# Performance work log

Hardware: AMD Instinct MI355X
Metric: run time of the kernel (lower is better)

Reference implementation:

```python
import jax, jax.numpy as jnp
import numpy as np

B, TE, TD, HE, HD = 4, 512, 256, 128, 256

def setup_inputs() -> dict:
    key = jax.random.key(0)
    k1, k2, k3, k4, k5 = jax.random.split(key, 5)
    return {
        "encoder_out_seq": jax.random.normal(k1, (B, TE, HE), dtype=jnp.float32),
        "decoder_out_seq": jax.random.normal(k2, (B, TD, HD), dtype=jnp.float32),
        "W_a": jax.random.normal(k3, (HE, HE), dtype=jnp.float32) * 0.05,
        "U_a": jax.random.normal(k4, (HD, HE), dtype=jnp.float32) * 0.05,
        "V_a": jax.random.normal(k5, (HE, 1), dtype=jnp.float32) * 0.05,
    }

def reference(encoder_out_seq, decoder_out_seq, W_a, U_a, V_a):
    # Bahdanau additive attention, fully parallel over decoder steps
    # (the original K.rnn scan has no true recurrence: each step is independent).
    Ws = jnp.einsum('bse,ef->bsf', encoder_out_seq, W_a)   # [B,Te,He]
    Uh = jnp.einsum('btd,df->btf', decoder_out_seq, U_a)   # [B,Td,He]
    # [B,Td,Te,He] additive score features
    feat = jnp.tanh(Ws[:, None, :, :] + Uh[:, :, None, :])
    e = jnp.einsum('btsf,f->bts', feat, V_a[:, 0])         # [B,Td,Te]
    e = jax.nn.softmax(e, axis=-1)                         # attention weights
    c = jnp.einsum('bts,bse->bte', e, encoder_out_seq)     # [B,Td,He] contexts
    return (c, e)
```

## Files before the change

kernel.cpp:

```cpp
#include <hip/hip_runtime.h>

#define Bn  4
#define TEn 512
#define TDn 256
#define HEn 128
#define HDn 256

__device__ __forceinline__ float tanh_fast(float x) {
    float e = __expf(2.0f * x);
    return 1.0f - 2.0f * __builtin_amdgcn_rcpf(e + 1.0f);
}

__global__ __launch_bounds__(512) void ws_gemm_kernel(
    const float* __restrict__ enc, const float* __restrict__ W,
    float* __restrict__ Ws)
{
    __shared__ __align__(16) float enc_lds[4 * HEn];
    const int tid = threadIdx.x;
    const int c   = tid & (HEn - 1);
    const int rl  = tid >> 7;
    const int r0  = blockIdx.x * 4;
    enc_lds[tid] = enc[r0 * HEn + tid];
    __syncthreads();
    const float* wc = W + c;
    const float* er = enc_lds + rl * HEn;
    float acc = 0.f;
    #pragma unroll 4
    for (int k = 0; k < HEn; k += 8) {
        float4 e0 = *(const float4*)(er + k);
        float4 e1 = *(const float4*)(er + k + 4);
        acc = fmaf(e0.x, wc[(k + 0) * HEn], acc);
        acc = fmaf(e0.y, wc[(k + 1) * HEn], acc);
        acc = fmaf(e0.z, wc[(k + 2) * HEn], acc);
        acc = fmaf(e0.w, wc[(k + 3) * HEn], acc);
        acc = fmaf(e1.x, wc[(k + 4) * HEn], acc);
        acc = fmaf(e1.y, wc[(k + 5) * HEn], acc);
        acc = fmaf(e1.z, wc[(k + 6) * HEn], acc);
        acc = fmaf(e1.w, wc[(k + 7) * HEn], acc);
    }
    Ws[(r0 + rl) * HEn + c] = acc;
}

__global__ __launch_bounds__(512, 4) void attn_kernel(
    const float* __restrict__ enc, const float* __restrict__ dec,
    const float* __restrict__ U, const float* __restrict__ V,
    const float* __restrict__ Ws, float* __restrict__ c_out,
    float* __restrict__ e_out)
{
    const int bp   = blockIdx.x;
    const int b    = bp >> 7;
    const int t0   = (bp & 127) * 2;
    const int bt0  = b * TDn + t0;
    const int tid  = threadIdx.x;
    const int lane = tid & 63;
    const int wave = tid >> 6;

    __shared__ __align__(16) float dec_lds[2 * HDn];
    __shared__ __align__(16) float uh0[HEn];
    __shared__ __align__(16) float uh1[HEn];
    __shared__ __align__(16) float part[32][HEn];
    __shared__ __align__(16) float sc0[TEn];
    __shared__ __align__(16) float sc1[TEn];
    __shared__ float redm[2][8];
    __shared__ float reds[2][8];

    dec_lds[tid] = dec[bt0 * HDn + tid];
    __syncthreads();

    {
        const int f = tid & 127;
        const int p = tid >> 7;
        const float* d0 = dec_lds + p * 64;
        const float* d1 = dec_lds + HDn + p * 64;
        const float* u  = U + (p * 64) * HEn + f;
        float a0 = 0.f, a1 = 0.f;
        #pragma unroll 8
        for (int k = 0; k < 64; ++k) {
            const float uk = u[k * HEn];
            a0 = fmaf(d0[k], uk, a0);
            a1 = fmaf(d1[k], uk, a1);
        }
        part[p][f]     = a0;
        part[4 + p][f] = a1;
    }
    __syncthreads();
    if (tid < HEn)
        uh0[tid] = part[0][tid] + part[1][tid] + part[2][tid] + part[3][tid];
    else if (tid < 2 * HEn) {
        const int f = tid - HEn;
        uh1[f] = part[4][f] + part[5][f] + part[6][f] + part[7][f];
    }
    __syncthreads();

    {
        const int s_sub = lane & 7;
        const int f0    = (lane >> 3) * 16;
        float4 vv[4], u0[4], u1[4];
        #pragma unroll
        for (int j = 0; j < 4; ++j) {
            vv[j] = *(const float4*)(V   + f0 + 4 * j);
            u0[j] = *(const float4*)(uh0 + f0 + 4 * j);
            u1[j] = *(const float4*)(uh1 + f0 + 4 * j);
        }
        const float* wsb = Ws + (b * TEn + wave * 64) * HEn;
        #pragma unroll 2
        for (int ci = 0; ci < 8; ++ci) {
            const float* wp = wsb + (ci * 8 + s_sub) * HEn + f0;
            float x0 = 0.f, x1 = 0.f;
            #pragma unroll
            for (int j = 0; j < 4; ++j) {
                float4 w = ((const float4*)wp)[j];
                x0 = fmaf(vv[j].x, tanh_fast(w.x + u0[j].x), x0);
                x1 = fmaf(vv[j].x, tanh_fast(w.x + u1[j].x), x1);
                x0 = fmaf(vv[j].y, tanh_fast(w.y + u0[j].y), x0);
                x1 = fmaf(vv[j].y, tanh_fast(w.y + u1[j].y), x1);
                x0 = fmaf(vv[j].z, tanh_fast(w.z + u0[j].z), x0);
                x1 = fmaf(vv[j].z, tanh_fast(w.z + u1[j].z), x1);
                x0 = fmaf(vv[j].w, tanh_fast(w.w + u0[j].w), x0);
                x1 = fmaf(vv[j].w, tanh_fast(w.w + u1[j].w), x1);
            }
            x0 += __shfl_xor(x0, 8, 64);
            x1 += __shfl_xor(x1, 8, 64);
            x0 += __shfl_xor(x0, 16, 64);
            x1 += __shfl_xor(x1, 16, 64);
            x0 += __shfl_xor(x0, 32, 64);
            x1 += __shfl_xor(x1, 32, 64);
            if (lane < 8) {
                sc0[wave * 64 + ci * 8 + lane] = x0;
                sc1[wave * 64 + ci * 8 + lane] = x1;
            }
        }
    }
    __syncthreads();

    const float v0 = sc0[tid];
    const float v1 = sc1[tid];
    float m0 = v0, m1 = v1;
    #pragma unroll
    for (int off = 32; off; off >>= 1) {
        m0 = fmaxf(m0, __shfl_xor(m0, off, 64));
        m1 = fmaxf(m1, __shfl_xor(m1, off, 64));
    }
    if (lane == 0) { redm[0][wave] = m0; redm[1][wave] = m1; }
    __syncthreads();
    float bm0 = redm[0][0], bm1 = redm[1][0];
    #pragma unroll
    for (int w = 1; w < 8; ++w) {
        bm0 = fmaxf(bm0, redm[0][w]);
        bm1 = fmaxf(bm1, redm[1][w]);
    }
    const float ex0 = __expf(v0 - bm0);
    const float ex1 = __expf(v1 - bm1);
    float s0 = ex0, s1 = ex1;
    #pragma unroll
    for (int off = 32; off; off >>= 1) {
        s0 += __shfl_xor(s0, off, 64);
        s1 += __shfl_xor(s1, off, 64);
    }
    if (lane == 0) { reds[0][wave] = s0; reds[1][wave] = s1; }
    __syncthreads();
    float bs0 = reds[0][0], bs1 = reds[1][0];
    #pragma unroll
    for (int w = 1; w < 8; ++w) { bs0 += reds[0][w]; bs1 += reds[1][w]; }
    const float e0 = ex0 * __builtin_amdgcn_rcpf(bs0);
    const float e1 = ex1 * __builtin_amdgcn_rcpf(bs1);
    e_out[bt0 * TEn + tid]       = e0;
    e_out[(bt0 + 1) * TEn + tid] = e1;
    sc0[tid] = e0;
    sc1[tid] = e1;
    __syncthreads();

    {
        const int hl = tid & 31;
        const int sp = tid >> 5;
        const float* eb = enc + (b * TEn + sp * 32) * HEn + hl * 4;
        const float* p0 = sc0 + sp * 32;
        const float* p1 = sc1 + sp * 32;
        float4 a0 = {0.f, 0.f, 0.f, 0.f};
        float4 a1 = {0.f, 0.f, 0.f, 0.f};
        #pragma unroll 4
        for (int i = 0; i < 32; ++i) {
            const float w0 = p0[i];
            const float w1 = p1[i];
            const float4 ev = *(const float4*)(eb + i * HEn);
            a0.x = fmaf(w0, ev.x, a0.x);  a1.x = fmaf(w1, ev.x, a1.x);
            a0.y = fmaf(w0, ev.y, a0.y);  a1.y = fmaf(w1, ev.y, a1.y);
            a0.z = fmaf(w0, ev.z, a0.z);  a1.z = fmaf(w1, ev.z, a1.z);
            a0.w = fmaf(w0, ev.w, a0.w);  a1.w = fmaf(w1, ev.w, a1.w);
        }
        *(float4*)&part[sp][hl * 4]      = a0;
        *(float4*)&part[16 + sp][hl * 4] = a1;
    }
    __syncthreads();
    if (tid < 2 * HEn) {
        const int tsel = tid >> 7;
        const int h    = tid & 127;
        float s = 0.f;
        #pragma unroll
        for (int p = 0; p < 16; ++p) s += part[tsel * 16 + p][h];
        c_out[(bt0 + tsel) * HEn + h] = s;
    }
}

extern "C" void kernel_launch(void* const* d_in, const int* in_sizes, int n_in,
                              void* d_out, int out_size, void* d_ws, size_t ws_size,
                              hipStream_t stream) {
    const float* enc = (const float*)d_in[0];
    const float* dec = (const float*)d_in[1];
    const float* W   = (const float*)d_in[2];
    const float* U   = (const float*)d_in[3];
    const float* V   = (const float*)d_in[4];
    float* out   = (float*)d_out;
    float* c_out = out;
    float* e_out = out + Bn * TDn * HEn;
    float* Ws    = (float*)d_ws;

    ws_gemm_kernel<<<(Bn * TEn) / 4, 512, 0, stream>>>(enc, W, Ws);
    attn_kernel<<<(Bn * TDn) / 2, 512, 0, stream>>>(enc, dec, U, V, Ws, c_out, e_out);
}
```

Measured before the change: 95.99 us.

## Process four decoder steps per block with 1024 threads to reuse Ws and enc loads

The attention kernel now handles four decoder timesteps per block instead of two, using 1024 threads and 256 blocks. Each loaded Ws and encoder element is reused across four query rows, which halves global and L2 traffic for those tensors per output. In exchange, each thread holds more registers (four accumulators, 16 float4 of Uh), and there are fewer, larger blocks. The partial-sum buffer grows to 64KB of LDS, which may limit occupancy and leave CUs underused.

```diff
diff --git a/kernel.cpp b/kernel.cpp
--- a/kernel.cpp
+++ b/kernel.cpp
@@ -41,28 +41,25 @@
     Ws[(r0 + rl) * HEn + c] = acc;
 }
 
-__global__ __launch_bounds__(512, 4) void attn_kernel(
+__global__ __launch_bounds__(1024, 4) void attn_kernel(
     const float* __restrict__ enc, const float* __restrict__ dec,
     const float* __restrict__ U, const float* __restrict__ V,
     const float* __restrict__ Ws, float* __restrict__ c_out,
     float* __restrict__ e_out)
 {
-    const int bp   = blockIdx.x;
-    const int b    = bp >> 7;
-    const int t0   = (bp & 127) * 2;
+    const int b    = blockIdx.x >> 6;
+    const int t0   = (blockIdx.x & 63) * 4;
     const int bt0  = b * TDn + t0;
     const int tid  = threadIdx.x;
     const int lane = tid & 63;
     const int wave = tid >> 6;
 
-    __shared__ __align__(16) float dec_lds[2 * HDn];
-    __shared__ __align__(16) float uh0[HEn];
-    __shared__ __align__(16) float uh1[HEn];
-    __shared__ __align__(16) float part[32][HEn];
-    __shared__ __align__(16) float sc0[TEn];
-    __shared__ __align__(16) float sc1[TEn];
-    __shared__ float redm[2][8];
-    __shared__ float reds[2][8];
+    __shared__ __align__(16) float dec_lds[4 * HDn];
+    __shared__ __align__(16) float uh[4][HEn];
+    __shared__ __align__(16) float sc[4][TEn];
+    __shared__ __align__(16) float part[32][512];
+    __shared__ float redm[4][8];
+    __shared__ float reds[4][8];
 
     dec_lds[tid] = dec[bt0 * HDn + tid];
     __syncthreads();
@@ -70,135 +67,156 @@
     {
         const int f = tid & 127;
         const int p = tid >> 7;
-        const float* d0 = dec_lds + p * 64;
-        const float* d1 = dec_lds + HDn + p * 64;
-        const float* u  = U + (p * 64) * HEn + f;
-        float a0 = 0.f, a1 = 0.f;
+        const float* u = U + (p * 32) * HEn + f;
+        float a0 = 0.f, a1 = 0.f, a2 = 0.f, a3 = 0.f;
         #pragma unroll 8
-        for (int k = 0; k < 64; ++k) {
+        for (int k = 0; k < 32; ++k) {
             const float uk = u[k * HEn];
-            a0 = fmaf(d0[k], uk, a0);
-            a1 = fmaf(d1[k], uk, a1);
-        }
-        part[p][f]     = a0;
-        part[4 + p][f] = a1;
-    }
-    __syncthreads();
-    if (tid < HEn)
-        uh0[tid] = part[0][tid] + part[1][tid] + part[2][tid] + part[3][tid];
-    else if (tid < 2 * HEn) {
-        const int f = tid - HEn;
-        uh1[f] = part[4][f] + part[5][f] + part[6][f] + part[7][f];
+            const int kk = p * 32 + k;
+            a0 = fmaf(dec_lds[kk],            uk, a0);
+            a1 = fmaf(dec_lds[HDn + kk],      uk, a1);
+            a2 = fmaf(dec_lds[2 * HDn + kk],  uk, a2);
+            a3 = fmaf(dec_lds[3 * HDn + kk],  uk, a3);
+        }
+        part[p][f]       = a0;
+        part[p][128 + f] = a1;
+        part[p][256 + f] = a2;
+        part[p][384 + f] = a3;
+    }
+    __syncthreads();
+    if (tid < 512) {
+        const int r = tid >> 7, f = tid & 127;
+        float s = 0.f;
+        #pragma unroll
+        for (int p = 0; p < 8; ++p) s += part[p][r * 128 + f];
+        uh[r][f] = s;
     }
     __syncthreads();
 
     {
         const int s_sub = lane & 7;
         const int f0    = (lane >> 3) * 16;
-        float4 vv[4], u0[4], u1[4];
+        float4 vv[4], uu[4][4];
         #pragma unroll
         for (int j = 0; j < 4; ++j) {
-            vv[j] = *(const float4*)(V   + f0 + 4 * j);
-            u0[j] = *(const float4*)(uh0 + f0 + 4 * j);
-            u1[j] = *(const float4*)(uh1 + f0 + 4 * j);
-        }
-        const float* wsb = Ws + (b * TEn + wave * 64) * HEn;
-        #pragma unroll 2
-        for (int ci = 0; ci < 8; ++ci) {
+            vv[j] = *(const float4*)(V + f0 + 4 * j);
+            #pragma unroll
+            for (int r = 0; r < 4; ++r)
+                uu[r][j] = *(const float4*)(&uh[r][f0 + 4 * j]);
+        }
+        const float* wsb = Ws + (b * TEn + wave * 32) * HEn;
+        #pragma unroll
+        for (int ci = 0; ci < 4; ++ci) {
             const float* wp = wsb + (ci * 8 + s_sub) * HEn + f0;
-            float x0 = 0.f, x1 = 0.f;
+            float x0 = 0.f, x1 = 0.f, x2 = 0.f, x3 = 0.f;
             #pragma unroll
             for (int j = 0; j < 4; ++j) {
                 float4 w = ((const float4*)wp)[j];
-                x0 = fmaf(vv[j].x, tanh_fast(w.x + u0[j].x), x0);
-                x1 = fmaf(vv[j].x, tanh_fast(w.x + u1[j].x), x1);
-                x0 = fmaf(vv[j].y, tanh_fast(w.y + u0[j].y), x0);
-                x1 = fmaf(vv[j].y, tanh_fast(w.y + u1[j].y), x1);
-                x0 = fmaf(vv[j].z, tanh_fast(w.z + u0[j].z), x0);
-                x1 = fmaf(vv[j].z, tanh_fast(w.z + u1[j].z), x1);
-                x0 = fmaf(vv[j].w, tanh_fast(w.w + u0[j].w), x0);
-                x1 = fmaf(vv[j].w, tanh_fast(w.w + u1[j].w), x1);
+                x0 = fmaf(vv[j].x, tanh_fast(w.x + uu[0][j].x), x0);
+                x1 = fmaf(vv[j].x, tanh_fast(w.x + uu[1][j].x), x1);
+                x2 = fmaf(vv[j].x, tanh_fast(w.x + uu[2][j].x), x2);
+                x3 = fmaf(vv[j].x, tanh_fast(w.x + uu[3][j].x), x3);
+                x0 = fmaf(vv[j].y, tanh_fast(w.y + uu[0][j].y), x0);
+                x1 = fmaf(vv[j].y, tanh_fast(w.y + uu[1][j].y), x1);
+                x2 = fmaf(vv[j].y, tanh_fast(w.y + uu[2][j].y), x2);
+                x3 = fmaf(vv[j].y, tanh_fast(w.y + uu[3][j].y), x3);
+                x0 = fmaf(vv[j].z, tanh_fast(w.z + uu[0][j].z), x0);
+                x1 = fmaf(vv[j].z, tanh_fast(w.z + uu[1][j].z), x1);
+                x2 = fmaf(vv[j].z, tanh_fast(w.z + uu[2][j].z), x2);
+                x3 = fmaf(vv[j].z, tanh_fast(w.z + uu[3][j].z), x3);
+                x0 = fmaf(vv[j].w, tanh_fast(w.w + uu[0][j].w), x0);
+                x1 = fmaf(vv[j].w, tanh_fast(w.w + uu[1][j].w), x1);
+                x2 = fmaf(vv[j].w, tanh_fast(w.w + uu[2][j].w), x2);
+                x3 = fmaf(vv[j].w, tanh_fast(w.w + uu[3][j].w), x3);
             }
-            x0 += __shfl_xor(x0, 8, 64);
-            x1 += __shfl_xor(x1, 8, 64);
-            x0 += __shfl_xor(x0, 16, 64);
-            x1 += __shfl_xor(x1, 16, 64);
-            x0 += __shfl_xor(x0, 32, 64);
-            x1 += __shfl_xor(x1, 32, 64);
+            x0 += __shfl_xor(x0, 8, 64);  x1 += __shfl_xor(x1, 8, 64);
+            x2 += __shfl_xor(x2, 8, 64);  x3 += __shfl_xor(x3, 8, 64);
+            x0 += __shfl_xor(x0, 16, 64); x1 += __shfl_xor(x1, 16, 64);
+            x2 += __shfl_xor(x2, 16, 64); x3 += __shfl_xor(x3, 16, 64);
+            x0 += __shfl_xor(x0, 32, 64); x1 += __shfl_xor(x1, 32, 64);
+            x2 += __shfl_xor(x2, 32, 64); x3 += __shfl_xor(x3, 32, 64);
             if (lane < 8) {
-                sc0[wave * 64 + ci * 8 + lane] = x0;
-                sc1[wave * 64 + ci * 8 + lane] = x1;
+                const int s = wave * 32 + ci * 8 + lane;
+                sc[0][s] = x0; sc[1][s] = x1; sc[2][s] = x2; sc[3][s] = x3;
             }
         }
     }
     __syncthreads();
 
-    const float v0 = sc0[tid];
-    const float v1 = sc1[tid];
-    float m0 = v0, m1 = v1;
-    #pragma unroll
-    for (int off = 32; off; off >>= 1) {
-        m0 = fmaxf(m0, __shfl_xor(m0, off, 64));
-        m1 = fmaxf(m1, __shfl_xor(m1, off, 64));
-    }
-    if (lane == 0) { redm[0][wave] = m0; redm[1][wave] = m1; }
-    __syncthreads();
-    float bm0 = redm[0][0], bm1 = redm[1][0];
-    #pragma unroll
-    for (int w = 1; w < 8; ++w) {
-        bm0 = fmaxf(bm0, redm[0][w]);
-        bm1 = fmaxf(bm1, redm[1][w]);
-    }
-    const float ex0 = __expf(v0 - bm0);
-    const float ex1 = __expf(v1 - bm1);
-    float s0 = ex0, s1 = ex1;
-    #pragma unroll
-    for (int off = 32; off; off >>= 1) {
-        s0 += __shfl_xor(s0, off, 64);
-        s1 += __shfl_xor(s1, off, 64);
-    }
-    if (lane == 0) { reds[0][wave] = s0; reds[1][wave] = s1; }
-    __syncthreads();
-    float bs0 = reds[0][0], bs1 = reds[1][0];
-    #pragma unroll
-    for (int w = 1; w < 8; ++w) { bs0 += reds[0][w]; bs1 += reds[1][w]; }
-    const float e0 = ex0 * __builtin_amdgcn_rcpf(bs0);
-    const float e1 = ex1 * __builtin_amdgcn_rcpf(bs1);
-    e_out[bt0 * TEn + tid]       = e0;
-    e_out[(bt0 + 1) * TEn + tid] = e1;
-    sc0[tid] = e0;
-    sc1[tid] = e1;
+    {
+        const int s  = tid & 511;
+        const int r0 = (tid >> 9) * 2;
+        const int w8 = wave & 7;
+        const float v0 = sc[r0][s];
+        const float v1 = sc[r0 + 1][s];
+        float m0 = v0, m1 = v1;
+        #pragma unroll
+        for (int off = 32; off; off >>= 1) {
+            m0 = fmaxf(m0, __shfl_xor(m0, off, 64));
+            m1 = fmaxf(m1, __shfl_xor(m1, off, 64));
+        }
+        if (lane == 0) { redm[r0][w8] = m0; redm[r0 + 1][w8] = m1; }
+        __syncthreads();
+        float bm0 = redm[r0][0], bm1 = redm[r0 + 1][0];
+        #pragma unroll
+        for (int w = 1; w < 8; ++w) {
+            bm0 = fmaxf(bm0, redm[r0][w]);
+            bm1 = fmaxf(bm1, redm[r0 + 1][w]);
+        }
+        const float ex0 = __expf(v0 - bm0);
+        const float ex1 = __expf(v1 - bm1);
+        float s0 = ex0, s1 = ex1;
+        #pragma unroll
+        for (int off = 32; off; off >>= 1) {
+            s0 += __shfl_xor(s0, off, 64);
+            s1 += __shfl_xor(s1, off, 64);
+        }
+        if (lane == 0) { reds[r0][w8] = s0; reds[r0 + 1][w8] = s1; }
+        __syncthreads();
+        float bs0 = reds[r0][0], bs1 = reds[r0 + 1][0];
+        #pragma unroll
+        for (int w = 1; w < 8; ++w) { bs0 += reds[r0][w]; bs1 += reds[r0 + 1][w]; }
+        const float e0 = ex0 * __builtin_amdgcn_rcpf(bs0);
+        const float e1 = ex1 * __builtin_amdgcn_rcpf(bs1);
+        e_out[(bt0 + r0) * TEn + s]     = e0;
+        e_out[(bt0 + r0 + 1) * TEn + s] = e1;
+        sc[r0][s]     = e0;
+        sc[r0 + 1][s] = e1;
+    }
     __syncthreads();
 
     {
         const int hl = tid & 31;
         const int sp = tid >> 5;
-        const float* eb = enc + (b * TEn + sp * 32) * HEn + hl * 4;
-        const float* p0 = sc0 + sp * 32;
-        const float* p1 = sc1 + sp * 32;
-        float4 a0 = {0.f, 0.f, 0.f, 0.f};
-        float4 a1 = {0.f, 0.f, 0.f, 0.f};
+        const float* eb = enc + (b * TEn + sp * 16) * HEn + hl * 4;
+        float4 a0 = {0,0,0,0}, a1 = {0,0,0,0}, a2 = {0,0,0,0}, a3 = {0,0,0,0};
         #pragma unroll 4
-        for (int i = 0; i < 32; ++i) {
-            const float w0 = p0[i];
-            const float w1 = p1[i];
+        for (int i = 0; i < 16; ++i) {
+            const int s = sp * 16 + i;
             const float4 ev = *(const float4*)(eb + i * HEn);
-            a0.x = fmaf(w0, ev.x, a0.x);  a1.x = fmaf(w1, ev.x, a1.x);
-            a0.y = fmaf(w0, ev.y, a0.y);  a1.y = fmaf(w1, ev.y, a1.y);
-            a0.z = fmaf(w0, ev.z, a0.z);  a1.z = fmaf(w1, ev.z, a1.z);
-            a0.w = fmaf(w0, ev.w, a0.w);  a1.w = fmaf(w1, ev.w, a1.w);
-        }
-        *(float4*)&part[sp][hl * 4]      = a0;
-        *(float4*)&part[16 + sp][hl * 4] = a1;
-    }
-    __syncthreads();
-    if (tid < 2 * HEn) {
-        const int tsel = tid >> 7;
-        const int h    = tid & 127;
+            const float w0 = sc[0][s], w1 = sc[1][s];
+            const float w2 = sc[2][s], w3 = sc[3][s];
+            a0.x = fmaf(w0, ev.x, a0.x); a1.x = fmaf(w1, ev.x, a1.x);
+            a2.x = fmaf(w2, ev.x, a2.x); a3.x = fmaf(w3, ev.x, a3.x);
+            a0.y = fmaf(w0, ev.y, a0.y); a1.y = fmaf(w1, ev.y, a1.y);
+            a2.y = fmaf(w2, ev.y, a2.y); a3.y = fmaf(w3, ev.y, a3.y);
+            a0.z = fmaf(w0, ev.z, a0.z); a1.z = fmaf(w1, ev.z, a1.z);
+            a2.z = fmaf(w2, ev.z, a2.z); a3.z = fmaf(w3, ev.z, a3.z);
+            a0.w = fmaf(w0, ev.w, a0.w); a1.w = fmaf(w1, ev.w, a1.w);
+            a2.w = fmaf(w2, ev.w, a2.w); a3.w = fmaf(w3, ev.w, a3.w);
+        }
+        *(float4*)&part[sp][0   + hl * 4] = a0;
+        *(float4*)&part[sp][128 + hl * 4] = a1;
+        *(float4*)&part[sp][256 + hl * 4] = a2;
+        *(float4*)&part[sp][384 + hl * 4] = a3;
+    }
+    __syncthreads();
+    if (tid < 512) {
+        const int r = tid >> 7, h = tid & 127;
         float s = 0.f;
         #pragma unroll
-        for (int p = 0; p < 16; ++p) s += part[tsel * 16 + p][h];
-        c_out[(bt0 + tsel) * HEn + h] = s;
+        for (int p = 0; p < 32; ++p) s += part[p][r * 128 + h];
+        c_out[(bt0 + r) * HEn + h] = s;
     }
 }
 
@@ -216,5 +234,5 @@
     float* Ws    = (float*)d_ws;
 
     ws_gemm_kernel<<<(Bn * TEn) / 4, 512, 0, stream>>>(enc, W, Ws);
-    attn_kernel<<<(Bn * TDn) / 2, 512, 0, stream>>>(enc, dec, U, V, Ws, c_out, e_out);
-}
+    attn_kernel<<<(Bn * TDn) / 4, 1024, 0, stream>>>(enc, dec, U, V, Ws, c_out, e_out);
+}
```

New measurement: 94.78 us. Within noise of the previous version (-1.3%).

## Split attention into prep, score and context kernels; precompute Uh in prep

Applied to the files above, without the earlier changes.

Moves the decoder projection Uh out of the per-block attention kernel into a combined prep kernel that computes both Ws and Uh, and splits the rest into a score/softmax kernel and a separate context kernel. The score kernel drops its large LDS partial buffer and declares a higher occupancy target, and tanh uses exp2 with a folded constant. The cost is an extra kernel launch and a write then reread of the attention weights through global memory.

```diff
diff --git a/kernel.cpp b/kernel.cpp
--- a/kernel.cpp
+++ b/kernel.cpp
@@ -7,90 +7,89 @@
 #define HDn 256
 
 __device__ __forceinline__ float tanh_fast(float x) {
-    float e = __expf(2.0f * x);
+    float e = __builtin_amdgcn_exp2f(x * 2.8853900817779268f);
     return 1.0f - 2.0f * __builtin_amdgcn_rcpf(e + 1.0f);
 }
 
-__global__ __launch_bounds__(512) void ws_gemm_kernel(
+__global__ __launch_bounds__(512) void prep_kernel(
     const float* __restrict__ enc, const float* __restrict__ W,
-    float* __restrict__ Ws)
+    const float* __restrict__ dec, const float* __restrict__ U,
+    float* __restrict__ Ws, float* __restrict__ Uh)
 {
-    __shared__ __align__(16) float enc_lds[4 * HEn];
+    __shared__ __align__(16) float lds[2048];
     const int tid = threadIdx.x;
-    const int c   = tid & (HEn - 1);
-    const int rl  = tid >> 7;
-    const int r0  = blockIdx.x * 4;
-    enc_lds[tid] = enc[r0 * HEn + tid];
-    __syncthreads();
-    const float* wc = W + c;
-    const float* er = enc_lds + rl * HEn;
-    float acc = 0.f;
-    #pragma unroll 4
-    for (int k = 0; k < HEn; k += 8) {
-        float4 e0 = *(const float4*)(er + k);
-        float4 e1 = *(const float4*)(er + k + 4);
-        acc = fmaf(e0.x, wc[(k + 0) * HEn], acc);
-        acc = fmaf(e0.y, wc[(k + 1) * HEn], acc);
-        acc = fmaf(e0.z, wc[(k + 2) * HEn], acc);
-        acc = fmaf(e0.w, wc[(k + 3) * HEn], acc);
-        acc = fmaf(e1.x, wc[(k + 4) * HEn], acc);
-        acc = fmaf(e1.y, wc[(k + 5) * HEn], acc);
-        acc = fmaf(e1.z, wc[(k + 6) * HEn], acc);
-        acc = fmaf(e1.w, wc[(k + 7) * HEn], acc);
-    }
-    Ws[(r0 + rl) * HEn + c] = acc;
-}
-
-__global__ __launch_bounds__(512, 4) void attn_kernel(
-    const float* __restrict__ enc, const float* __restrict__ dec,
-    const float* __restrict__ U, const float* __restrict__ V,
-    const float* __restrict__ Ws, float* __restrict__ c_out,
-    float* __restrict__ e_out)
+    if (blockIdx.x < 256) {
+        const int r0 = blockIdx.x * 8;
+        *(float2*)&lds[2 * tid] = *(const float2*)(enc + r0 * HEn + 2 * tid);
+        __syncthreads();
+        const int c2 = (tid & 63) * 2;
+        const int rl = tid >> 6;
+        const float* er = lds + rl * HEn;
+        float a0 = 0.f, a1 = 0.f;
+        #pragma unroll 4
+        for (int k = 0; k < HEn; k += 4) {
+            const float4 e4 = *(const float4*)(er + k);
+            const float2 w0 = *(const float2*)(W + (k + 0) * HEn + c2);
+            const float2 w1 = *(const float2*)(W + (k + 1) * HEn + c2);
+            const float2 w2 = *(const float2*)(W + (k + 2) * HEn + c2);
+            const float2 w3 = *(const float2*)(W + (k + 3) * HEn + c2);
+            a0 = fmaf(e4.x, w0.x, a0); a1 = fmaf(e4.x, w0.y, a1);
+            a0 = fmaf(e4.y, w1.x, a0); a1 = fmaf(e4.y, w1.y, a1);
+            a0 = fmaf(e4.z, w2.x, a0); a1 = fmaf(e4.z, w2.y, a1);
+            a0 = fmaf(e4.w, w3.x, a0); a1 = fmaf(e4.w, w3.y, a1);
+        }
+        float2 o; o.x = a0; o.y = a1;
+        *(float2*)(Ws + (r0 + rl) * HEn + c2) = o;
+    } else {
+        const int r0 = (blockIdx.x - 256) * 4;
+        *(float2*)&lds[2 * tid] = *(const float2*)(dec + r0 * HDn + 2 * tid);
+        __syncthreads();
+        const int f2 = (tid & 63) * 2;
+        const int rl = (tid >> 6) & 3;
+        const int kp = tid >> 8;
+        const float* d = lds + rl * HDn + kp * 128;
+        float a0 = 0.f, a1 = 0.f;
+        #pragma unroll 4
+        for (int k = 0; k < 128; k += 4) {
+            const float4 d4 = *(const float4*)(d + k);
+            const float2 u0 = *(const float2*)(U + (kp * 128 + k + 0) * HEn + f2);
+            const float2 u1 = *(const float2*)(U + (kp * 128 + k + 1) * HEn + f2);
+            const float2 u2 = *(const float2*)(U + (kp * 128 + k + 2) * HEn + f2);
+            const float2 u3 = *(const float2*)(U + (kp * 128 + k + 3) * HEn + f2);
+            a0 = fmaf(d4.x, u0.x, a0); a1 = fmaf(d4.x, u0.y, a1);
+            a0 = fmaf(d4.y, u1.x, a0); a1 = fmaf(d4.y, u1.y, a1);
+            a0 = fmaf(d4.z, u2.x, a0); a1 = fmaf(d4.z, u2.y, a1);
+            a0 = fmaf(d4.w, u3.x, a0); a1 = fmaf(d4.w, u3.y, a1);
+        }
+        __syncthreads();
+        __shared__ float part[2][4][HEn];
+        part[kp][rl][f2]     = a0;
+        part[kp][rl][f2 + 1] = a1;
+        __syncthreads();
+        if (kp == 0) {
+            float2 o;
+            o.x = part[0][rl][f2]     + part[1][rl][f2];
+            o.y = part[0][rl][f2 + 1] + part[1][rl][f2 + 1];
+            *(float2*)(Uh + (r0 + rl) * HEn + f2) = o;
+        }
+    }
+}
+
+__global__ __launch_bounds__(512, 6) void score_kernel(
+    const float* __restrict__ V, const float* __restrict__ Ws,
+    const float* __restrict__ Uh, float* __restrict__ e_out)
 {
     const int bp   = blockIdx.x;
     const int b    = bp >> 7;
-    const int t0   = (bp & 127) * 2;
-    const int bt0  = b * TDn + t0;
+    const int bt0  = b * TDn + (bp & 127) * 2;
     const int tid  = threadIdx.x;
     const int lane = tid & 63;
     const int wave = tid >> 6;
 
-    __shared__ __align__(16) float dec_lds[2 * HDn];
-    __shared__ __align__(16) float uh0[HEn];
-    __shared__ __align__(16) float uh1[HEn];
-    __shared__ __align__(16) float part[32][HEn];
     __shared__ __align__(16) float sc0[TEn];
     __shared__ __align__(16) float sc1[TEn];
     __shared__ float redm[2][8];
     __shared__ float reds[2][8];
-
-    dec_lds[tid] = dec[bt0 * HDn + tid];
-    __syncthreads();
-
-    {
-        const int f = tid & 127;
-        const int p = tid >> 7;
-        const float* d0 = dec_lds + p * 64;
-        const float* d1 = dec_lds + HDn + p * 64;
-        const float* u  = U + (p * 64) * HEn + f;
-        float a0 = 0.f, a1 = 0.f;
-        #pragma unroll 8
-        for (int k = 0; k < 64; ++k) {
-            const float uk = u[k * HEn];
-            a0 = fmaf(d0[k], uk, a0);
-            a1 = fmaf(d1[k], uk, a1);
-        }
-        part[p][f]     = a0;
-        part[4 + p][f] = a1;
-    }
-    __syncthreads();
-    if (tid < HEn)
-        uh0[tid] = part[0][tid] + part[1][tid] + part[2][tid] + part[3][tid];
-    else if (tid < 2 * HEn) {
-        const int f = tid - HEn;
-        uh1[f] = part[4][f] + part[5][f] + part[6][f] + part[7][f];
-    }
-    __syncthreads();
 
     {
         const int s_sub = lane & 7;
@@ -98,9 +97,9 @@
         float4 vv[4], u0[4], u1[4];
         #pragma unroll
         for (int j = 0; j < 4; ++j) {
-            vv[j] = *(const float4*)(V   + f0 + 4 * j);
-            u0[j] = *(const float4*)(uh0 + f0 + 4 * j);
-            u1[j] = *(const float4*)(uh1 + f0 + 4 * j);
+            vv[j] = *(const float4*)(V + f0 + 4 * j);
+            u0[j] = *(const float4*)(Uh + bt0 * HEn + f0 + 4 * j);
+            u1[j] = *(const float4*)(Uh + (bt0 + 1) * HEn + f0 + 4 * j);
         }
         const float* wsb = Ws + (b * TEn + wave * 64) * HEn;
         #pragma unroll 2
@@ -162,43 +161,49 @@
     float bs0 = reds[0][0], bs1 = reds[1][0];
     #pragma unroll
     for (int w = 1; w < 8; ++w) { bs0 += reds[0][w]; bs1 += reds[1][w]; }
-    const float e0 = ex0 * __builtin_amdgcn_rcpf(bs0);
-    const float e1 = ex1 * __builtin_amdgcn_rcpf(bs1);
-    e_out[bt0 * TEn + tid]       = e0;
-    e_out[(bt0 + 1) * TEn + tid] = e1;
-    sc0[tid] = e0;
-    sc1[tid] = e1;
-    __syncthreads();
-
-    {
-        const int hl = tid & 31;
-        const int sp = tid >> 5;
-        const float* eb = enc + (b * TEn + sp * 32) * HEn + hl * 4;
-        const float* p0 = sc0 + sp * 32;
-        const float* p1 = sc1 + sp * 32;
-        float4 a0 = {0.f, 0.f, 0.f, 0.f};
-        float4 a1 = {0.f, 0.f, 0.f, 0.f};
-        #pragma unroll 4
-        for (int i = 0; i < 32; ++i) {
-            const float w0 = p0[i];
-            const float w1 = p1[i];
-            const float4 ev = *(const float4*)(eb + i * HEn);
-            a0.x = fmaf(w0, ev.x, a0.x);  a1.x = fmaf(w1, ev.x, a1.x);
-            a0.y = fmaf(w0, ev.y, a0.y);  a1.y = fmaf(w1, ev.y, a1.y);
-            a0.z = fmaf(w0, ev.z, a0.z);  a1.z = fmaf(w1, ev.z, a1.z);
-            a0.w = fmaf(w0, ev.w, a0.w);  a1.w = fmaf(w1, ev.w, a1.w);
-        }
-        *(float4*)&part[sp][hl * 4]      = a0;
-        *(float4*)&part[16 + sp][hl * 4] = a1;
-    }
+    e_out[bt0 * TEn + tid]       = ex0 * __builtin_amdgcn_rcpf(bs0);
+    e_out[(bt0 + 1) * TEn + tid] = ex1 * __builtin_amdgcn_rcpf(bs1);
+}
+
+__global__ __launch_bounds__(512, 4) void ctx_kernel(
+    const float* __restrict__ enc, const float* __restrict__ e_out,
+    float* __restrict__ c_out)
+{
+    const int bp  = blockIdx.x;
+    const int b   = bp >> 7;
+    const int bt0 = b * TDn + (bp & 127) * 2;
+    const int tid = threadIdx.x;
+
+    __shared__ __align__(16) float e_lds[2][TEn];
+    __shared__ __align__(16) float part[16][2 * HEn];
+
+    e_lds[0][tid] = e_out[bt0 * TEn + tid];
+    e_lds[1][tid] = e_out[(bt0 + 1) * TEn + tid];
+    __syncthreads();
+
+    const int hl = tid & 31;
+    const int sp = tid >> 5;
+    const float* eb = enc + (b * TEn + sp * 32) * HEn + hl * 4;
+    float4 a0 = {0,0,0,0}, a1 = {0,0,0,0};
+    #pragma unroll 4
+    for (int i = 0; i < 32; ++i) {
+        const int s = sp * 32 + i;
+        const float4 ev = *(const float4*)(eb + i * HEn);
+        const float w0 = e_lds[0][s], w1 = e_lds[1][s];
+        a0.x = fmaf(w0, ev.x, a0.x); a1.x = fmaf(w1, ev.x, a1.x);
+        a0.y = fmaf(w0, ev.y, a0.y); a1.y = fmaf(w1, ev.y, a1.y);
+        a0.z = fmaf(w0, ev.z, a0.z); a1.z = fmaf(w1, ev.z, a1.z);
+        a0.w = fmaf(w0, ev.w, a0.w); a1.w = fmaf(w1, ev.w, a1.w);
+    }
+    *(float4*)&part[sp][hl * 4]       = a0;
+    *(float4*)&part[sp][HEn + hl * 4] = a1;
     __syncthreads();
     if (tid < 2 * HEn) {
-        const int tsel = tid >> 7;
-        const int h    = tid & 127;
+        const int r = tid >> 7, h = tid & 127;
         float s = 0.f;
         #pragma unroll
-        for (int p = 0; p < 16; ++p) s += part[tsel * 16 + p][h];
-        c_out[(bt0 + tsel) * HEn + h] = s;
+        for (int p = 0; p < 16; ++p) s += part[p][r * HEn + h];
+        c_out[(bt0 + r) * HEn + h] = s;
     }
 }
 
@@ -214,7 +219,9 @@
     float* c_out = out;
     float* e_out = out + Bn * TDn * HEn;
     float* Ws    = (float*)d_ws;
-
-    ws_gemm_kernel<<<(Bn * TEn) / 4, 512, 0, stream>>>(enc, W, Ws);
-    attn_kernel<<<(Bn * TDn) / 2, 512, 0, stream>>>(enc, dec, U, V, Ws, c_out, e_out);
-}
+    float* Uh    = (float*)d_ws + Bn * TEn * HEn;
+
+    prep_kernel<<<512, 512, 0, stream>>>(enc, W, dec, U, Ws, Uh);
+    score_kernel<<<Bn * TDn / 2, 512, 0, stream>>>(V, Ws, Uh, e_out);
+    ctx_kernel<<<Bn * TDn / 2, 512, 0, stream>>>(enc, e_out, c_out);
+}
```

Result: slower. 107.2 us (+11.6%).
